# Kernel optimization log

Hardware: AMD Instinct MI355X
Metric: run time of the kernel (lower is better)

Reference implementation:

```python
import jax, jax.numpy as jnp
import numpy as np

D_MODEL = 512
N_HEADS = 8
HEAD_DIM = D_MODEL // N_HEADS          # 64
ROTARY_DIM = HEAD_DIM // 2             # 32 (rotary_frac = 0.5)
MAX_SEQ_LEN = 512
EPS = 1e-6


def _rope_tables(seq_len, dtype=jnp.float32):
    inv_freq = 1.0 / (10000.0 ** (jnp.arange(0, ROTARY_DIM, 2, dtype=jnp.float32) / ROTARY_DIM))
    t = jnp.arange(seq_len, dtype=jnp.float32)
    freqs = jnp.outer(t, inv_freq)          # (T, ROTARY_DIM//2)
    return jnp.sin(freqs).astype(dtype), jnp.cos(freqs).astype(dtype)


def _apply_rope(x, sin, cos):
    # x: (R, H, T, Dh); rotate interleaved pairs of the first ROTARY_DIM dims
    rd = ROTARY_DIM
    x1 = x[..., :rd].reshape(*x.shape[:-1], rd // 2, 2)
    x2 = x[..., rd:]
    s = sin[None, None, :, :]
    c = cos[None, None, :, :]
    a, b = x1[..., 0], x1[..., 1]
    rot = jnp.stack([a * c - b * s, a * s + b * c], axis=-1).reshape(*x.shape[:-1], rd)
    return jnp.concatenate([rot, x2], axis=-1)


def setup_inputs() -> dict:
    key = jax.random.key(0)
    ks = jax.random.split(key, 8)
    B, T, N, D = 1, 384, 128, D_MODEL
    x = jax.random.normal(ks[0], (B, T, N, D), dtype=jnp.float32)
    neuron_pad_mask = jax.random.randint(ks[1], (B, N), 0, 2, dtype=jnp.int32)
    scale = 1.0 / np.sqrt(D)
    norm_w = jnp.ones((D,), dtype=jnp.float32)
    wq = jax.random.normal(ks[2], (D, D), dtype=jnp.float32) * scale
    wk = jax.random.normal(ks[3], (D, D), dtype=jnp.float32) * scale
    wv = jax.random.normal(ks[4], (D, D), dtype=jnp.float32) * scale
    wo = jax.random.normal(ks[5], (D, D), dtype=jnp.float32) * scale
    return {"x": x, "neuron_pad_mask": neuron_pad_mask, "norm_w": norm_w,
            "wq": wq, "wk": wk, "wv": wv, "wo": wo}


def reference(x, neuron_pad_mask, norm_w, wq, wk, wv, wo):
    B, T, N, D = x.shape
    H, Dh = N_HEADS, HEAD_DIM

    # RMSNorm over d_model
    xn = x * jax.lax.rsqrt(jnp.mean(x * x, axis=-1, keepdims=True) + EPS) * norm_w

    # (B,T,N,D) -> (B*N, T, D): each neuron is an independent causal timeline
    xt = jnp.transpose(xn, (0, 2, 1, 3)).reshape(B * N, T, D)
    res = xt

    # QKV projections (Linear, no bias: x @ W^T), split into heads -> (R,H,T,Dh)
    def to_bhld(y):
        return jnp.transpose(y.reshape(B * N, T, H, Dh), (0, 2, 1, 3))

    q = to_bhld(xt @ wq.T)
    k = to_bhld(xt @ wk.T)
    v = to_bhld(xt @ wv.T)

    sin, cos = _rope_tables(T, dtype=x.dtype)
    q = _apply_rope(q, sin, cos)
    k = _apply_rope(k, sin, cos)

    # Causal SDPA per row (scale = 1/sqrt(Dh), matching F.scaled_dot_product_attention)
    scores = jnp.einsum('rhtd,rhsd->rhts', q, k) / np.sqrt(Dh).astype(x.dtype)
    causal = jnp.tril(jnp.ones((T, T), dtype=bool))
    scores = jnp.where(causal[None, None], scores, jnp.finfo(scores.dtype).min)
    attn = jax.nn.softmax(scores, axis=-1)
    out = jnp.einsum('rhts,rhsd->rhtd', attn, v)            # (R,H,T,Dh)
    out = jnp.transpose(out, (0, 2, 1, 3)).reshape(B * N, T, D)

    # Only valid (non-padded) neuron rows receive attention output (others stay 0)
    valid = (neuron_pad_mask.reshape(-1) != 0)
    out = jnp.where(valid[:, None, None], out, jnp.zeros((), dtype=out.dtype))

    out = out + res
    out = jnp.transpose(out.reshape(B, N, T, D), (0, 2, 1, 3))  # (B,T,N,D)
    return out @ wo.T
```

## Files before the change

### kernel.cpp

```cpp
#include <hip/hip_runtime.h>
#include <hip/hip_bf16.h>
#include <stdint.h>

typedef __bf16 bf16x8 __attribute__((ext_vector_type(8)));
typedef float f32x4 __attribute__((ext_vector_type(4)));

static constexpr int T_SEQ  = 384;
static constexpr int NNEUR  = 128;
static constexpr int DMODEL = 512;
static constexpr int NROWS  = NNEUR * T_SEQ;
static constexpr float ROPE_C = 0.8304820237218406f;

__device__ __forceinline__ float bf2f(unsigned short u) {
  union { unsigned int i; float f; } x; x.i = ((unsigned int)u) << 16; return x.f;
}
__device__ __forceinline__ unsigned short f2bf(float f) {
  union { float f; unsigned int i; } x; x.f = f;
  unsigned int i = x.i;
  i += 0x7FFFu + ((i >> 16) & 1u);
  return (unsigned short)(i >> 16);
}
__device__ __forceinline__ float fast_exp2(float x) {
#if __has_builtin(__builtin_amdgcn_exp2f)
  return __builtin_amdgcn_exp2f(x);
#else
  return exp2f(x);
#endif
}

__device__ __forceinline__ void async_copy16(const unsigned short* g, unsigned short* l) {
  auto gp = reinterpret_cast<const __attribute__((address_space(1))) unsigned int*>(
      reinterpret_cast<uintptr_t>(g));
  auto lp = reinterpret_cast<__attribute__((address_space(3))) unsigned int*>(
      reinterpret_cast<uintptr_t>(l));
  __builtin_amdgcn_global_load_lds(gp, lp, 16, 0, 0);
}

__global__ __launch_bounds__(256) void cvt_w_kernel(
    const float* __restrict__ w0, const float* __restrict__ w1,
    const float* __restrict__ w2, const float* __restrict__ w3,
    unsigned short* __restrict__ o0, unsigned short* __restrict__ o1,
    unsigned short* __restrict__ o2, unsigned short* __restrict__ o3)
{
  const float* w; unsigned short* o;
  switch (blockIdx.y) {
    case 0:  w = w0; o = o0; break;
    case 1:  w = w1; o = o1; break;
    case 2:  w = w2; o = o2; break;
    default: w = w3; o = o3; break;
  }
  int i = (blockIdx.x * 256 + threadIdx.x) * 4;
  float4 v = *reinterpret_cast<const float4*>(w + i);
  union { unsigned short u[4]; uint2 v2; } p;
  p.u[0] = f2bf(v.x); p.u[1] = f2bf(v.y); p.u[2] = f2bf(v.z); p.u[3] = f2bf(v.w);
  *reinterpret_cast<uint2*>(o + i) = p.v2;
}

__global__ __launch_bounds__(256) void rope_tab_kernel(float2* __restrict__ tab) {
  int idx = blockIdx.x * 256 + threadIdx.x;
  int t = idx >> 4, i = idx & 15;
  float ang = (float)t * exp2f(-(float)i * ROPE_C);
  float s, c; sincosf(ang, &s, &c);
  tab[idx] = make_float2(s, c);
}

__global__ __launch_bounds__(256) void rmsnorm_kernel(
    const float* __restrict__ x, const float* __restrict__ nw,
    unsigned short* __restrict__ xt)
{
  int wave = threadIdx.x >> 6, lane = threadIdx.x & 63;
  int rid = blockIdx.x * 4 + wave;
  int t = rid >> 7, n = rid & 127;
  const float* row = x + (size_t)rid * DMODEL;
  float4 v0 = *reinterpret_cast<const float4*>(row + lane * 8);
  float4 v1 = *reinterpret_cast<const float4*>(row + lane * 8 + 4);
  float ss = v0.x*v0.x + v0.y*v0.y + v0.z*v0.z + v0.w*v0.w
           + v1.x*v1.x + v1.y*v1.y + v1.z*v1.z + v1.w*v1.w;
  #pragma unroll
  for (int off = 32; off; off >>= 1) ss += __shfl_xor(ss, off);
  float sc = rsqrtf(ss * (1.0f / DMODEL) + 1e-6f);
  float4 w0 = *reinterpret_cast<const float4*>(nw + lane * 8);
  float4 w1 = *reinterpret_cast<const float4*>(nw + lane * 8 + 4);
  union { unsigned short u[8]; uint4 v; } p;
  p.u[0] = f2bf(v0.x * sc * w0.x); p.u[1] = f2bf(v0.y * sc * w0.y);
  p.u[2] = f2bf(v0.z * sc * w0.z); p.u[3] = f2bf(v0.w * sc * w0.w);
  p.u[4] = f2bf(v1.x * sc * w1.x); p.u[5] = f2bf(v1.y * sc * w1.y);
  p.u[6] = f2bf(v1.z * sc * w1.z); p.u[7] = f2bf(v1.w * sc * w1.w);
  *reinterpret_cast<uint4*>(xt + ((size_t)n * T_SEQ + t) * DMODEL + lane * 8) = p.v;
}

template <int MODE, typename OutT>
__global__ __launch_bounds__(512, 4) void gemm_k(
    const unsigned short* __restrict__ A,
    const unsigned short* __restrict__ B,
    OutT* __restrict__ C,
    const float2* __restrict__ tab,
    const int* __restrict__ pad)
{
  __shared__ alignas(16) unsigned short Sh[2][12288];
  const int tid  = threadIdx.x;
  const int wave = tid >> 6, lane = tid & 63;
  const int l15  = lane & 15, quad = lane >> 4;
  const int wm = (wave >> 1) * 64, wn = (wave & 1) * 64;

  constexpr int GX = (MODE == 2) ? 8 : (MODE == 3) ? 2 : 4;
  constexpr int GY = (MODE == 3) ? 384 : 192;
  constexpr int NB = GX * GY;
  constexpr int CH = NB / 8;
  const int lin = (int)blockIdx.y * GX + (int)blockIdx.x;
  const int swz = (lin & 7) * CH + (lin >> 3);
  const int bx  = swz % GX, by = swz / GX;

  size_t m0; int n0;
  if constexpr (MODE == 3) { m0 = (size_t)bx * 256; n0 = by * 128; }
  else                     { m0 = (size_t)by * 256; n0 = bx * 128; }

  if constexpr (MODE == 2) {
    int nfirst = (int)(m0 / 384);
    int nlast  = (int)((m0 + 255) / 384);
    if (pad[nfirst] == 0 && pad[nlast] == 0) return;
  }
  if constexpr (MODE == 3) {
    if (pad[n0 / 384] == 0) return;
  }

  const int r4 = tid >> 2;
  const int c4 = tid & 3;
  const int gc = c4 ^ (r4 & 3);
  const unsigned short* ga = A + (m0 + r4) * 512 + gc * 8;
  const unsigned short* gb = B + ((size_t)n0 + r4) * 512 + gc * 8;

  const int pc = (quad ^ (l15 & 3)) * 8;

  auto STAGE = [&](int kk, int b) {
    const unsigned short* gak = ga + kk * 32;
    unsigned short* base = &Sh[b][0];
    async_copy16(gak,             base + tid * 8);
    async_copy16(gak + 128 * 512, base + 4096 + tid * 8);
    async_copy16(gb + kk * 32,    base + 8192 + tid * 8);
  };

  f32x4 acc[4][4] = {};
  auto COMPUTE = [&](int b) {
    const unsigned short* base = &Sh[b][0];
    bf16x8 a[4], bb[4];
    #pragma unroll
    for (int i = 0; i < 4; ++i)
      a[i] = *reinterpret_cast<const bf16x8*>(&base[(wm + i * 16 + l15) * 32 + pc]);
    #pragma unroll
    for (int j = 0; j < 4; ++j)
      bb[j] = *reinterpret_cast<const bf16x8*>(&base[8192 + (wn + j * 16 + l15) * 32 + pc]);
    #pragma unroll
    for (int i = 0; i < 4; ++i)
      #pragma unroll
      for (int j = 0; j < 4; ++j)
        acc[i][j] = __builtin_amdgcn_mfma_f32_16x16x32_bf16(a[i], bb[j], acc[i][j], 0, 0, 0);
  };

  STAGE(0, 0);
  #pragma unroll 2
  for (int kk = 0; kk < 15; ++kk) {
    const int b = kk & 1;
    STAGE(kk + 1, b ^ 1);
    asm volatile("s_waitcnt vmcnt(3)" ::: "memory");
    __builtin_amdgcn_s_barrier();
    __builtin_amdgcn_sched_barrier(0);
    COMPUTE(b);
    __builtin_amdgcn_sched_barrier(0);
    __builtin_amdgcn_s_barrier();
    __builtin_amdgcn_sched_barrier(0);
  }
  asm volatile("s_waitcnt vmcnt(0)" ::: "memory");
  __builtin_amdgcn_s_barrier();
  __builtin_amdgcn_sched_barrier(0);
  COMPUTE(1);

  if constexpr (MODE == 3) {
    #pragma unroll
    for (int j = 0; j < 4; ++j) {
      int xbase = n0 + wn + j * 16;
      int nn    = xbase / 384;
      int bloc  = xbase - nn * 384;
      int off64 = (bloc >> 6) * 64 + ((bloc >> 4) & 3);
      #pragma unroll
      for (int i = 0; i < 4; ++i)
        #pragma unroll
        for (int r = 0; r < 4; ++r) {
          int dout = (int)m0 + wm + i * 16 + quad * 4 + r;
          C[((size_t)nn * 512 + dout) * 384 + off64 + l15 * 4] = f2bf(acc[i][j][r]);
        }
    }
  } else {
    OutT* Cb = C;
    int ncol0 = n0 + wn;
    if constexpr (MODE == 2) {
      int sec = n0 >> 9;
      Cb = C + (size_t)sec * NROWS * 512;
      ncol0 = (n0 & 511) + wn;
    }
    #pragma unroll
    for (int i = 0; i < 4; ++i) {
      #pragma unroll
      for (int r = 0; r < 4; ++r) {
        size_t grow = m0 + wm + i * 16 + quad * 4 + r;
        int t = (int)(grow % 384);
        #pragma unroll
        for (int j = 0; j < 4; ++j) {
          float v = acc[i][j][r];
          int col = ncol0 + j * 16 + l15;
          if constexpr (MODE == 2) {
            if (((ncol0 + j * 16) & 63) < 32) {
              float part = __shfl_xor(v, 1);
              float2 scv = tab[t * 16 + ((col & 63) >> 1)];
              v = (l15 & 1) ? (part * scv.x + v * scv.y)
                            : (v * scv.y - part * scv.x);
            }
            Cb[grow * 512 + col] = f2bf(v);
          } else {
            Cb[grow * 512 + col] = v;
          }
        }
      }
    }
  }
}

__global__ __launch_bounds__(256, 4) void attn_kernel(
    const unsigned short* __restrict__ qb,
    const unsigned short* __restrict__ kb,
    const unsigned short* __restrict__ vt,
    const unsigned short* __restrict__ xt,
    const int* __restrict__ pad,
    unsigned short* __restrict__ y)
{
  const int lin = (int)blockIdx.x + 3 * ((int)blockIdx.y + 8 * (int)blockIdx.z);
  const int swz = (lin & 7) * 384 + (lin >> 3);
  const int qtb = swz % 3;
  const int rem = swz / 3;
  const int h   = rem & 7;
  const int n   = rem >> 3;

  const int tid  = threadIdx.x;

  if (pad[n] == 0) {
    int rb = tid >> 2;
    int d  = h * 64 + (tid & 3) * 16;
    #pragma unroll
    for (int rr = 0; rr < 128; rr += 64) {
      int tq = qtb * 128 + rr + rb;
      const uint4* src = reinterpret_cast<const uint4*>(
          &xt[((size_t)n * T_SEQ + tq) * 512 + d]);
      uint4* dst = reinterpret_cast<uint4*>(
          &y[((size_t)tq * NNEUR + n) * 512 + d]);
      dst[0] = src[0];
      dst[1] = src[1];
    }
    return;
  }

  __shared__ alignas(16) unsigned short Qs[128 * 64];
  __shared__ alignas(16) unsigned short Ks[64 * 64];
  __shared__ alignas(16) unsigned short VTs[64 * 64];
  __shared__ alignas(16) unsigned short Ps[4][16][72];

  const int wave = tid >> 6, lane = tid & 63;
  const int l15  = lane & 15, quad = lane >> 4;
  const int lrow = lane >> 3, lchunk = (lane & 7) ^ ((lane >> 3) & 7);
  const float C2 = 0.18033688011112042f;

  const unsigned short* gq =
      qb + ((size_t)n * T_SEQ + qtb * 128 + wave * 32 + lrow) * 512 + h * 64 + lchunk * 8;
  #pragma unroll
  for (int rr = 0; rr < 4; ++rr)
    async_copy16(gq + (size_t)(rr * 8) * 512, &Qs[(wave * 32 + rr * 8) * 64]);

  const unsigned short* gk0 =
      kb + ((size_t)n * T_SEQ + wave * 16 + lrow) * 512 + h * 64 + lchunk * 8;
  const unsigned short* gv0 =
      vt + ((size_t)n * 512 + h * 64 + wave * 16 + lrow) * 384 + lchunk * 8;

  const int nkt = 2 * qtb + 2;

  float lsum[2][4] = {};
  f32x4 oacc[2][4] = {};

  async_copy16(gk0,           &Ks[(wave * 16) * 64]);
  async_copy16(gk0 + 8 * 512, &Ks[(wave * 16 + 8) * 64]);
  async_copy16(gv0,           &VTs[(wave * 16) * 64]);
  async_copy16(gv0 + 8 * 384, &VTs[(wave * 16 + 8) * 64]);
  __syncthreads();

  bf16x8 aq[2][2];
  #pragma unroll
  for (int s = 0; s < 2; ++s)
    #pragma unroll
    for (int kc = 0; kc < 2; ++kc) {
      const int pcq = ((kc * 4 + quad) ^ (l15 & 7)) * 8;
      aq[s][kc] = *reinterpret_cast<const bf16x8*>(
          &Qs[(wave * 32 + s * 16 + l15) * 64 + pcq]);
    }

  for (int kt = 0; kt < nkt; ++kt) {
    #pragma unroll
    for (int s = 0; s < 2; ++s) {
      const int qsub = qtb * 128 + wave * 32 + s * 16;
      if (kt * 64 > qsub + 15) continue;

      f32x4 sc4[4] = {};
      #pragma unroll
      for (int kc = 0; kc < 2; ++kc) {
        const int pc = ((kc * 4 + quad) ^ (l15 & 7)) * 8;
        #pragma unroll
        for (int tc = 0; tc < 4; ++tc) {
          bf16x8 bk = *reinterpret_cast<const bf16x8*>(&Ks[(tc * 16 + l15) * 64 + pc]);
          sc4[tc] = __builtin_amdgcn_mfma_f32_16x16x32_bf16(aq[s][kc], bk, sc4[tc], 0, 0, 0);
        }
      }
      float ps_[4][4];
      #pragma unroll
      for (int tc = 0; tc < 4; ++tc)
        #pragma unroll
        for (int r = 0; r < 4; ++r) {
          float p = fast_exp2(sc4[tc][r] * C2 - 16.0f);
          int kglob = kt * 64 + tc * 16 + l15;
          int qglob = qsub + quad * 4 + r;
          if (kglob > qglob) p = 0.f;
          lsum[s][r] += p;
          ps_[tc][r] = p;
        }
      #pragma unroll
      for (int r = 0; r < 4; ++r) {
        union { float f; unsigned int u; } a0, a1, a2, a3;
        a0.f = ps_[0][r]; a1.f = ps_[1][r]; a2.f = ps_[2][r]; a3.f = ps_[3][r];
        uint2 pk;
        pk.x = (a1.u & 0xffff0000u) | (a0.u >> 16);
        pk.y = (a3.u & 0xffff0000u) | (a2.u >> 16);
        *reinterpret_cast<uint2*>(&Ps[wave][quad * 4 + r][l15 * 4]) = pk;
      }
      #pragma unroll
      for (int kc = 0; kc < 2; ++kc) {
        const int pc = ((kc * 4 + quad) ^ (l15 & 7)) * 8;
        bf16x8 ap = *reinterpret_cast<const bf16x8*>(&Ps[wave][l15][kc * 32 + quad * 8]);
        #pragma unroll
        for (int dt = 0; dt < 4; ++dt) {
          bf16x8 bv = *reinterpret_cast<const bf16x8*>(&VTs[(dt * 16 + l15) * 64 + pc]);
          oacc[s][dt] = __builtin_amdgcn_mfma_f32_16x16x32_bf16(ap, bv, oacc[s][dt], 0, 0, 0);
        }
      }
    }
    if (kt + 1 < nkt) {
      __syncthreads();
      const size_t ko = (size_t)(kt + 1) * 64;
      async_copy16(gk0 + ko * 512,                 &Ks[(wave * 16) * 64]);
      async_copy16(gk0 + (ko + 8) * 512,           &Ks[(wave * 16 + 8) * 64]);
      async_copy16(gv0 + (kt + 1) * 64,            &VTs[(wave * 16) * 64]);
      async_copy16(gv0 + (kt + 1) * 64 + 8 * 384,  &VTs[(wave * 16 + 8) * 64]);
      __syncthreads();
    }
  }

  float inv[2][4];
  #pragma unroll
  for (int s = 0; s < 2; ++s)
    #pragma unroll
    for (int r = 0; r < 4; ++r) {
      float l = lsum[s][r];
      l += __shfl_xor(l, 1);
      l += __shfl_xor(l, 2);
      l += __shfl_xor(l, 4);
      l += __shfl_xor(l, 8);
      inv[s][r] = 1.0f / l;
    }
  #pragma unroll
  for (int s = 0; s < 2; ++s)
    #pragma unroll
    for (int dt = 0; dt < 4; ++dt)
      #pragma unroll
      for (int r = 0; r < 4; ++r) {
        int tq = qtb * 128 + wave * 32 + s * 16 + quad * 4 + r;
        int d  = h * 64 + dt * 16 + l15;
        float val = oacc[s][dt][r] * inv[s][r];
        float res = bf2f(xt[((size_t)n * T_SEQ + tq) * 512 + d]);
        y[((size_t)tq * NNEUR + n) * 512 + d] = f2bf(val + res);
      }
}

extern "C" void kernel_launch(void* const* d_in, const int* in_sizes, int n_in,
                              void* d_out, int out_size, void* d_ws, size_t ws_size,
                              hipStream_t stream) {
  const float* x   = (const float*)d_in[0];
  const int*   pad = (const int*)d_in[1];
  const float* nw  = (const float*)d_in[2];
  const float* wq  = (const float*)d_in[3];
  const float* wk  = (const float*)d_in[4];
  const float* wv  = (const float*)d_in[5];
  const float* wo  = (const float*)d_in[6];
  float* out = (float*)d_out;

  char* ws = (char*)d_ws;
  size_t off = 0;
  auto alloc = [&](size_t bytes) { void* p = ws + off; off += (bytes + 255) & ~(size_t)255; return p; };
  const size_t WELEM  = (size_t)512 * 512;
  const size_t MBYTES = (size_t)NROWS * 512 * 2;
  unsigned short* wqkv_bf = (unsigned short*)alloc(WELEM * 3 * 2);
  unsigned short* wo_bf   = (unsigned short*)alloc(WELEM * 2);
  float2*         rtab    = (float2*)alloc(384 * 16 * sizeof(float2));
  unsigned short* xt_bf   = (unsigned short*)alloc(MBYTES);
  unsigned short* qk_buf  = (unsigned short*)alloc(MBYTES * 2);
  unsigned short* vt_buf  = (unsigned short*)alloc(MBYTES);
  unsigned short* y_buf   = (unsigned short*)alloc(MBYTES);

  cvt_w_kernel<<<dim3(256, 4), 256, 0, stream>>>(
      wq, wk, wv, wo,
      wqkv_bf, wqkv_bf + WELEM, wqkv_bf + 2 * WELEM, wo_bf);
  rope_tab_kernel<<<24, 256, 0, stream>>>(rtab);
  rmsnorm_kernel<<<NROWS / 4, 256, 0, stream>>>(x, nw, xt_bf);
  gemm_k<2, unsigned short><<<dim3(8, NROWS / 256), 512, 0, stream>>>(
      xt_bf, wqkv_bf, qk_buf, rtab, pad);
  gemm_k<3, unsigned short><<<dim3(2, NROWS / 128), 512, 0, stream>>>(
      wqkv_bf + 2 * WELEM, xt_bf, vt_buf, nullptr, pad);
  attn_kernel<<<dim3(3, 8, 128), 256, 0, stream>>>(
      qk_buf, qk_buf + (size_t)NROWS * 512, vt_buf, xt_bf, pad, y_buf);
  gemm_k<0, float><<<dim3(4, NROWS / 256), 512, 0, stream>>>(
      y_buf, wo_bf, out, nullptr, pad);
}
```

Baseline: 347.9 us.

## Shrink GEMM tiles to 128x128 with single-buffered BK=64 and fuse prep kernels

The GEMM kernel moves from 256x128 tiles with 512 threads and a double-buffered BK=32 async pipeline to 128x128 tiles with 256 threads, a single LDS buffer and BK=64 with an 8-way XOR swizzle. Smaller tiles let padded-neuron blocks be skipped more precisely and raise the block count. In exchange, global-to-LDS loads no longer overlap with MFMA compute. The rope table generation is also folded into the weight conversion kernel, removing one launch.

Result: no change. 342.0 us (-1.7%).

```diff
diff --git a/kernel.cpp b/kernel.cpp
--- a/kernel.cpp
+++ b/kernel.cpp
@@ -36,12 +36,22 @@
   __builtin_amdgcn_global_load_lds(gp, lp, 16, 0, 0);
 }
 
-__global__ __launch_bounds__(256) void cvt_w_kernel(
+__global__ __launch_bounds__(256) void prep_kernel(
     const float* __restrict__ w0, const float* __restrict__ w1,
     const float* __restrict__ w2, const float* __restrict__ w3,
     unsigned short* __restrict__ o0, unsigned short* __restrict__ o1,
-    unsigned short* __restrict__ o2, unsigned short* __restrict__ o3)
+    unsigned short* __restrict__ o2, unsigned short* __restrict__ o3,
+    float2* __restrict__ tab)
 {
+  if (blockIdx.y == 4) {
+    if (blockIdx.x >= 24) return;
+    int idx = blockIdx.x * 256 + threadIdx.x;
+    int t = idx >> 4, i = idx & 15;
+    float ang = (float)t * exp2f(-(float)i * ROPE_C);
+    float s, c; sincosf(ang, &s, &c);
+    tab[idx] = make_float2(s, c);
+    return;
+  }
   const float* w; unsigned short* o;
   switch (blockIdx.y) {
     case 0:  w = w0; o = o0; break;
@@ -54,14 +64,6 @@
   union { unsigned short u[4]; uint2 v2; } p;
   p.u[0] = f2bf(v.x); p.u[1] = f2bf(v.y); p.u[2] = f2bf(v.z); p.u[3] = f2bf(v.w);
   *reinterpret_cast<uint2*>(o + i) = p.v2;
-}
-
-__global__ __launch_bounds__(256) void rope_tab_kernel(float2* __restrict__ tab) {
-  int idx = blockIdx.x * 256 + threadIdx.x;
-  int t = idx >> 4, i = idx & 15;
-  float ang = (float)t * exp2f(-(float)i * ROPE_C);
-  float s, c; sincosf(ang, &s, &c);
-  tab[idx] = make_float2(s, c);
 }
 
 __global__ __launch_bounds__(256) void rmsnorm_kernel(
@@ -90,21 +92,21 @@
 }
 
 template <int MODE, typename OutT>
-__global__ __launch_bounds__(512, 4) void gemm_k(
+__global__ __launch_bounds__(256, 4) void gemm_k(
     const unsigned short* __restrict__ A,
     const unsigned short* __restrict__ B,
     OutT* __restrict__ C,
     const float2* __restrict__ tab,
     const int* __restrict__ pad)
 {
-  __shared__ alignas(16) unsigned short Sh[2][12288];
+  __shared__ alignas(16) unsigned short Sh[256 * 64];
   const int tid  = threadIdx.x;
   const int wave = tid >> 6, lane = tid & 63;
   const int l15  = lane & 15, quad = lane >> 4;
   const int wm = (wave >> 1) * 64, wn = (wave & 1) * 64;
 
-  constexpr int GX = (MODE == 2) ? 8 : (MODE == 3) ? 2 : 4;
-  constexpr int GY = (MODE == 3) ? 384 : 192;
+  constexpr int GX = (MODE == 2) ? 8 : 4;
+  constexpr int GY = 384;
   constexpr int NB = GX * GY;
   constexpr int CH = NB / 8;
   const int lin = (int)blockIdx.y * GX + (int)blockIdx.x;
@@ -112,68 +114,48 @@
   const int bx  = swz % GX, by = swz / GX;
 
   size_t m0; int n0;
-  if constexpr (MODE == 3) { m0 = (size_t)bx * 256; n0 = by * 128; }
-  else                     { m0 = (size_t)by * 256; n0 = bx * 128; }
+  if constexpr (MODE == 3) { m0 = (size_t)bx * 128; n0 = by * 128; }
+  else                     { m0 = (size_t)by * 128; n0 = bx * 128; }
 
   if constexpr (MODE == 2) {
-    int nfirst = (int)(m0 / 384);
-    int nlast  = (int)((m0 + 255) / 384);
-    if (pad[nfirst] == 0 && pad[nlast] == 0) return;
+    if (pad[(int)(m0 / 384)] == 0) return;
   }
   if constexpr (MODE == 3) {
     if (pad[n0 / 384] == 0) return;
   }
 
-  const int r4 = tid >> 2;
-  const int c4 = tid & 3;
-  const int gc = c4 ^ (r4 & 3);
-  const unsigned short* ga = A + (m0 + r4) * 512 + gc * 8;
-  const unsigned short* gb = B + ((size_t)n0 + r4) * 512 + gc * 8;
-
-  const int pc = (quad ^ (l15 & 3)) * 8;
-
-  auto STAGE = [&](int kk, int b) {
-    const unsigned short* gak = ga + kk * 32;
-    unsigned short* base = &Sh[b][0];
-    async_copy16(gak,             base + tid * 8);
-    async_copy16(gak + 128 * 512, base + 4096 + tid * 8);
-    async_copy16(gb + kk * 32,    base + 8192 + tid * 8);
-  };
+  const int r0 = tid >> 3;
+  const int gc = (tid & 7) ^ (r0 & 7);
+  const unsigned short* ga = A + (m0 + r0) * 512 + gc * 8;
+  const unsigned short* gb = B + ((size_t)n0 + r0) * 512 + gc * 8;
+  unsigned short* ls = &Sh[tid * 8];
 
   f32x4 acc[4][4] = {};
-  auto COMPUTE = [&](int b) {
-    const unsigned short* base = &Sh[b][0];
-    bf16x8 a[4], bb[4];
-    #pragma unroll
-    for (int i = 0; i < 4; ++i)
-      a[i] = *reinterpret_cast<const bf16x8*>(&base[(wm + i * 16 + l15) * 32 + pc]);
-    #pragma unroll
-    for (int j = 0; j < 4; ++j)
-      bb[j] = *reinterpret_cast<const bf16x8*>(&base[8192 + (wn + j * 16 + l15) * 32 + pc]);
-    #pragma unroll
-    for (int i = 0; i < 4; ++i)
+  for (int k0 = 0; k0 < 512; k0 += 64) {
+    #pragma unroll
+    for (int rr = 0; rr < 4; ++rr) {
+      async_copy16(ga + (size_t)rr * 32 * 512 + k0, ls + rr * 2048);
+      async_copy16(gb + (size_t)rr * 32 * 512 + k0, ls + 8192 + rr * 2048);
+    }
+    __syncthreads();
+    #pragma unroll
+    for (int kc = 0; kc < 2; ++kc) {
+      const int pc = ((kc * 4 + quad) ^ (l15 & 7)) * 8;
+      bf16x8 a[4], b[4];
+      #pragma unroll
+      for (int i = 0; i < 4; ++i)
+        a[i] = *reinterpret_cast<const bf16x8*>(&Sh[(wm + i * 16 + l15) * 64 + pc]);
       #pragma unroll
       for (int j = 0; j < 4; ++j)
-        acc[i][j] = __builtin_amdgcn_mfma_f32_16x16x32_bf16(a[i], bb[j], acc[i][j], 0, 0, 0);
-  };
-
-  STAGE(0, 0);
-  #pragma unroll 2
-  for (int kk = 0; kk < 15; ++kk) {
-    const int b = kk & 1;
-    STAGE(kk + 1, b ^ 1);
-    asm volatile("s_waitcnt vmcnt(3)" ::: "memory");
-    __builtin_amdgcn_s_barrier();
-    __builtin_amdgcn_sched_barrier(0);
-    COMPUTE(b);
-    __builtin_amdgcn_sched_barrier(0);
-    __builtin_amdgcn_s_barrier();
-    __builtin_amdgcn_sched_barrier(0);
-  }
-  asm volatile("s_waitcnt vmcnt(0)" ::: "memory");
-  __builtin_amdgcn_s_barrier();
-  __builtin_amdgcn_sched_barrier(0);
-  COMPUTE(1);
+        b[j] = *reinterpret_cast<const bf16x8*>(&Sh[(128 + wn + j * 16 + l15) * 64 + pc]);
+      #pragma unroll
+      for (int i = 0; i < 4; ++i)
+        #pragma unroll
+        for (int j = 0; j < 4; ++j)
+          acc[i][j] = __builtin_amdgcn_mfma_f32_16x16x32_bf16(a[i], b[j], acc[i][j], 0, 0, 0);
+    }
+    __syncthreads();
+  }
 
   if constexpr (MODE == 3) {
     #pragma unroll
@@ -410,17 +392,16 @@
   unsigned short* vt_buf  = (unsigned short*)alloc(MBYTES);
   unsigned short* y_buf   = (unsigned short*)alloc(MBYTES);
 
-  cvt_w_kernel<<<dim3(256, 4), 256, 0, stream>>>(
+  prep_kernel<<<dim3(256, 5), 256, 0, stream>>>(
       wq, wk, wv, wo,
-      wqkv_bf, wqkv_bf + WELEM, wqkv_bf + 2 * WELEM, wo_bf);
-  rope_tab_kernel<<<24, 256, 0, stream>>>(rtab);
+      wqkv_bf, wqkv_bf + WELEM, wqkv_bf + 2 * WELEM, wo_bf, rtab);
   rmsnorm_kernel<<<NROWS / 4, 256, 0, stream>>>(x, nw, xt_bf);
-  gemm_k<2, unsigned short><<<dim3(8, NROWS / 256), 512, 0, stream>>>(
+  gemm_k<2, unsigned short><<<dim3(8, NROWS / 128), 256, 0, stream>>>(
       xt_bf, wqkv_bf, qk_buf, rtab, pad);
-  gemm_k<3, unsigned short><<<dim3(2, NROWS / 128), 512, 0, stream>>>(
+  gemm_k<3, unsigned short><<<dim3(4, NROWS / 128), 256, 0, stream>>>(
       wqkv_bf + 2 * WELEM, xt_bf, vt_buf, nullptr, pad);
   attn_kernel<<<dim3(3, 8, 128), 256, 0, stream>>>(
       qk_buf, qk_buf + (size_t)NROWS * 512, vt_buf, xt_bf, pad, y_buf);
-  gemm_k<0, float><<<dim3(4, NROWS / 256), 512, 0, stream>>>(
+  gemm_k<0, float><<<dim3(4, NROWS / 128), 256, 0, stream>>>(
       y_buf, wo_bf, out, nullptr, pad);
 }
```
